# Performance work log

Hardware: AMD Instinct MI355X
Metric: run time of the kernel (lower is better)

Reference implementation:

```python
import jax, jax.numpy as jnp
import numpy as np


def _blur_kernel():
    # make_kernel([1,3,3,1]) -> outer product, normalized; * upsample_factor**2 (=4)
    k = np.array([1.0, 3.0, 3.0, 1.0], dtype=np.float32)
    k2 = np.outer(k, k)
    k2 /= k2.sum()
    k2 *= 4.0
    return jnp.asarray(k2)  # [4,4]


def setup_inputs() -> dict:
    key = jax.random.key(0)
    ks = jax.random.split(key, 6)
    B, Cin, Cout, H, W = 8, 128, 128, 128, 128
    style_dim, sd = 512, 32
    lin_out = Cin * (sd // 2) * (sd // 2)  # 128*16*16 = 32768
    return {
        "x": jax.random.normal(ks[0], (B, Cin, H, W), jnp.float32),
        "style": jax.random.normal(ks[1], (B, style_dim), jnp.float32),
        "weight": jax.random.normal(ks[2], (Cout, Cin, 3, 3), jnp.float32),
        "lin_w": jax.random.normal(ks[3], (lin_out, style_dim), jnp.float32),
        "lin_b": jnp.ones((lin_out,), jnp.float32),  # bias_init=1
        "convw_w": jax.random.normal(ks[4], (Cout, Cin, 3, 3), jnp.float32),
        "convw_b": jnp.zeros((Cout,), jnp.float32),
        "convb_w": jax.random.normal(ks[5], (Cout, Cin, 3, 3), jnp.float32),
        "convb_b": jnp.zeros((Cout,), jnp.float32),
    }


DN = ('NCHW', 'OIHW', 'NCHW')


def reference(x, style, weight, lin_w, lin_b, convw_w, convw_b, convb_w, convb_b):
    B, Cin, H, W = x.shape
    Cout, K = weight.shape[0], weight.shape[2]
    scale = 1.0 / np.sqrt(Cin * K * K)  # equalized-lr scale, fan_in = Cin*K*K
    w = scale * weight  # [Cout, Cin, K, K]; identical per-sample -> plain conv

    # F.conv_transpose2d(stride=2, padding=0) == dilated conv with flipped kernel
    out = jax.lax.conv_general_dilated(
        x, jnp.flip(w, (2, 3)), (1, 1), [(K - 1, K - 1)] * 2,
        lhs_dilation=(2, 2), dimension_numbers=DN)  # [B, Cout, 2H+1, 2W+1]

    # upfirdn2d blur with pad=(1,1): depthwise conv with flipped 4x4 kernel
    bk = _blur_kernel()
    bw = jnp.tile(jnp.flip(bk, (0, 1))[None, None], (Cout, 1, 1, 1))  # [Cout,1,4,4]
    out = jax.lax.conv_general_dilated(
        out, bw, (1, 1), [(1, 1), (1, 1)], feature_group_count=Cout,
        dimension_numbers=DN)  # [B, Cout, 2H, 2W]

    # InstanceNorm2d(affine=False), eps=1e-5, biased variance
    mu = out.mean((2, 3), keepdims=True)
    var = out.var((2, 3), keepdims=True)
    out = (out - mu) * jax.lax.rsqrt(var + 1e-5)
    Ho, Wo = out.shape[2], out.shape[3]

    # spatial_modulation_shared: EqualLinear (fused_lrelu) + View
    half = int(round(np.sqrt(lin_w.shape[0] // Cin)))  # spatial_dim // 2
    sd = 2 * half
    lscale = 1.0 / np.sqrt(style.shape[1])
    s = style @ (lin_w * lscale).T
    s = jax.nn.leaky_relu(s + lin_b, 0.2) * np.sqrt(2.0)  # fused_leaky_relu
    smap = s.reshape(B, Cin, half, half)
    # nn.Upsample(scale_factor=2, mode='nearest')
    smap = jnp.repeat(jnp.repeat(smap, 2, axis=2), 2, axis=3)  # [B,Cin,sd,sd]

    # two EqualConv2d(Cin, Cout, 3, padding=1)
    cscale = 1.0 / np.sqrt(Cin * 9)
    sw = jax.lax.conv_general_dilated(smap, convw_w * cscale, (1, 1),
                                      [(1, 1), (1, 1)], dimension_numbers=DN)
    sw = sw + convw_b[None, :, None, None]
    sb = jax.lax.conv_general_dilated(smap, convb_w * cscale, (1, 1),
                                      [(1, 1), (1, 1)], dimension_numbers=DN)
    sb = sb + convb_b[None, :, None, None]

    # F.interpolate(mode='nearest') to (Ho, Wo)
    hi = jnp.arange(Ho) * sd // Ho
    wi = jnp.arange(Wo) * sd // Wo
    sw = sw[:, :, hi][:, :, :, wi]
    sb = sb[:, :, hi][:, :, :, wi]

    return out * (1.0 + 0.3 * sw) + 0.3 * sb
```

## Files before the change

kernel.cpp:

```cpp
#include <hip/hip_runtime.h>
#include <cstdint>

#define SCALE_MAIN 0.029462782549439483f
#define LSCALE     0.044194173824159223f
#define CSCALE     0.029462782549439483f

typedef __attribute__((ext_vector_type(8))) short bf16x8;
typedef __attribute__((ext_vector_type(4))) float f32x4;
typedef __attribute__((ext_vector_type(4))) unsigned int u32x4;

static __device__ __forceinline__ float lrelu_s2(float v) {
  return (v > 0.f ? v : 0.2f * v) * 1.4142135623730951f;
}

static __device__ __forceinline__ unsigned short f2bf(float f) {
  unsigned int u = __builtin_bit_cast(unsigned int, f);
  u += 0x7FFFu + ((u >> 16) & 1u);
  return (unsigned short)(u >> 16);
}

__global__ __launch_bounds__(256) void keffb_kernel(const float* __restrict__ weight,
                                                    short* __restrict__ kb) {
  int idx = blockIdx.x * 256 + threadIdx.x;
  if (idx >= 128 * 128 * 36) return;
  int tap = idx % 9;
  int tmp = idx / 9;
  int par = tmp & 3;
  int cc  = tmp >> 2;
  int co = cc >> 7, ci = cc & 127;
  int ph = par >> 1, pw = par & 1;
  int a = tap / 3, b = tap % 3;
  int th = ph ? 3 - 2 * a : 2 - 2 * a;
  int tw = pw ? 3 - 2 * b : 2 - 2 * b;
  const float k4[4] = {1.f, 3.f, 3.f, 1.f};
  const float* wp = weight + cc * 9;
  float acc = 0.f;
  #pragma unroll
  for (int u = 0; u < 4; ++u) {
    int m = th - 1 + u;
    if (m < 0 || m > 2) continue;
    #pragma unroll
    for (int v = 0; v < 4; ++v) {
      int n = tw - 1 + v;
      if (n < 0 || n > 2) continue;
      acc += (k4[3 - u] * k4[3 - v] * (1.f / 16.f)) * wp[m * 3 + n];
    }
  }
  kb[(((par * 144) + tap * 16 + (ci >> 3)) * 128 + co) * 8 + (ci & 7)] =
      (short)f2bf(acc * SCALE_MAIN);
}

__global__ __launch_bounds__(256) void kb2_kernel(const float* __restrict__ cw_w,
                                                  const float* __restrict__ cb_w,
                                                  short* __restrict__ kb2) {
  int idx = blockIdx.x * 256 + threadIdx.x;
  if (idx >= 524288) return;
  int j   = idx & 7;
  int co  = (idx >> 3) & 255;
  int kc  = (idx >> 11) & 63;
  int par = idx >> 17;
  int k = kc * 8 + j;
  int t2 = k >> 7, ci = k & 127;
  int dy2 = t2 >> 1, dx2 = t2 & 1;
  int ph = par >> 1, pw = par & 1;
  const float* wsrc = (co < 128)
      ? cw_w + ((size_t)co * 128 + ci) * 9
      : cb_w + ((size_t)(co - 128) * 128 + ci) * 9;
  float acc = 0.f;
  #pragma unroll
  for (int kh = 0; kh < 3; ++kh) {
    bool okh = dy2 == 0 ? (ph == 0 ? kh == 0 : kh <= 1)
                        : (ph == 0 ? kh >= 1 : kh == 2);
    if (!okh) continue;
    #pragma unroll
    for (int kw = 0; kw < 3; ++kw) {
      bool okw = dx2 == 0 ? (pw == 0 ? kw == 0 : kw <= 1)
                          : (pw == 0 ? kw >= 1 : kw == 2);
      if (okw) acc += wsrc[kh * 3 + kw];
    }
  }
  kb2[idx] = (short)f2bf(acc * CSCALE);
}

__global__ __launch_bounds__(256) void xpose_kernel(const float* __restrict__ x,
                                                    unsigned short* __restrict__ xt) {
  int y = blockIdx.x, b = blockIdx.y;
  __shared__ unsigned short tl[128 * 134];
  int t = threadIdx.x;
  #pragma unroll 4
  for (int i = 0; i < 16; ++i) {
    int c = t + i * 256;
    int ci = c >> 5, x4 = c & 31;
    f32x4 v = *(const f32x4*)(x + (size_t)(b * 128 + ci) * 16384 + y * 128 + x4 * 4);
    unsigned int* dst = (unsigned int*)(tl + ci * 134 + x4 * 4);
    dst[0] = (unsigned int)f2bf(v.x) | ((unsigned int)f2bf(v.y) << 16);
    dst[1] = (unsigned int)f2bf(v.z) | ((unsigned int)f2bf(v.w) << 16);
  }
  __syncthreads();
  #pragma unroll 2
  for (int i = 0; i < 8; ++i) {
    int c = t + i * 256;
    int xcol = c >> 4, sub = c & 15;
    unsigned short u[8];
    #pragma unroll
    for (int j = 0; j < 8; ++j) u[j] = tl[(sub * 8 + j) * 134 + xcol];
    u32x4 o;
    o.x = (unsigned int)u[0] | ((unsigned int)u[1] << 16);
    o.y = (unsigned int)u[2] | ((unsigned int)u[3] << 16);
    o.z = (unsigned int)u[4] | ((unsigned int)u[5] << 16);
    o.w = (unsigned int)u[6] | ((unsigned int)u[7] << 16);
    *(u32x4*)(xt + ((size_t)(b * 128 + y) * 128 + xcol) * 128 + sub * 8) = o;
  }
}

__global__ __launch_bounds__(256) void style_kernel(const float* __restrict__ style,
                                                    const float* __restrict__ lin_w,
                                                    const float* __restrict__ lin_b,
                                                    unsigned short* __restrict__ smap_bf) {
  int wid = threadIdx.x >> 6, lane = threadIdx.x & 63;
  int gw = blockIdx.x * 4 + wid;
  const float4* st4 = (const float4*)style;
  float s[8][8];
  #pragma unroll
  for (int b = 0; b < 8; ++b) {
    float4 a0 = st4[b * 128 + lane * 2];
    float4 a1 = st4[b * 128 + lane * 2 + 1];
    s[b][0] = a0.x; s[b][1] = a0.y; s[b][2] = a0.z; s[b][3] = a0.w;
    s[b][4] = a1.x; s[b][5] = a1.y; s[b][6] = a1.z; s[b][7] = a1.w;
  }
  for (int rr = 0; rr < 16; ++rr) {
    int j = gw * 16 + rr;
    const float4* wp = (const float4*)(lin_w + (size_t)j * 512);
    float4 w0 = wp[lane * 2], w1 = wp[lane * 2 + 1];
    float acc[8];
    #pragma unroll
    for (int b = 0; b < 8; ++b) {
      acc[b] = w0.x * s[b][0] + w0.y * s[b][1] + w0.z * s[b][2] + w0.w * s[b][3]
             + w1.x * s[b][4] + w1.y * s[b][5] + w1.z * s[b][6] + w1.w * s[b][7];
    }
    #pragma unroll
    for (int m = 32; m; m >>= 1) {
      #pragma unroll
      for (int b = 0; b < 8; ++b) acc[b] += __shfl_xor(acc[b], m, 64);
    }
    if (lane == 0) {
      float bias = lin_b[j];
      int ci = j >> 8, sp = j & 255;
      #pragma unroll
      for (int b = 0; b < 8; ++b)
        smap_bf[(size_t)(b * 256 + sp) * 128 + ci] =
            f2bf(lrelu_s2(acc[b] * LSCALE + bias));
    }
  }
}

__global__ __launch_bounds__(512, 2) void modconv_kernel(
    const unsigned short* __restrict__ smap_bf, const short* __restrict__ kb2,
    const float* __restrict__ cw_b, const float* __restrict__ cb_b,
    float* __restrict__ swp) {
  extern __shared__ __align__(16) char dsm[];
  int par = blockIdx.x, b = blockIdx.y;
  int ph = par >> 1, pw = par & 1;
  int t = threadIdx.x, lane = t & 63, w = t >> 6;
  int q = w >> 1, ch = w & 1;
  int m15 = lane & 15, ksub = lane >> 4;

  for (int c = t; c < 4624; c += 512) {
    int s = c >> 4, cch = c & 15;
    int rr = s / 17, cc = s - rr * 17;
    int gr = rr - 1 + ph, gc = cc - 1 + pw;
    u32x4 v = {0u, 0u, 0u, 0u};
    if ((unsigned)gr < 16u && (unsigned)gc < 16u)
      v = *(const u32x4*)(smap_bf + ((size_t)(b * 256 + gr * 16 + gc) * 128 + cch * 8));
    int phys = (cch + s) & 15;
    *(u32x4*)(dsm + s * 256 + phys * 16) = v;
  }
  __syncthreads();

  const bf16x8* kbv = (const bf16x8*)kb2;
  f32x4 acc[4][8];
  #pragma unroll
  for (int i = 0; i < 4; ++i)
  #pragma unroll
  for (int j = 0; j < 8; ++j) acc[i][j] = (f32x4){0.f, 0.f, 0.f, 0.f};

  for (int s = 0; s < 16; ++s) {
    int t2 = s >> 2, dy2 = t2 >> 1, dx2 = t2 & 1;
    int cch = (s & 3) * 4 + ksub;
    bf16x8 av[4];
    #pragma unroll
    for (int mf = 0; mf < 4; ++mf) {
      int i = q * 4 + mf;
      int ssp = (i + dy2) * 17 + (m15 + dx2);
      int phys = (cch + ssp) & 15;
      av[mf] = *(const bf16x8*)(dsm + ssp * 256 + phys * 16);
    }
    #pragma unroll
    for (int nf = 0; nf < 8; ++nf) {
      bf16x8 bv = kbv[(size_t)((par * 64 + s * 4 + ksub) * 256 + ch * 128 + nf * 16 + m15)];
      #pragma unroll
      for (int mf = 0; mf < 4; ++mf)
        acc[mf][nf] = __builtin_amdgcn_mfma_f32_16x16x32_bf16(av[mf], bv, acc[mf][nf], 0, 0, 0);
    }
  }

  int jbase = ksub * 4;
  #pragma unroll
  for (int nf = 0; nf < 8; ++nf) {
    int co = ch * 128 + nf * 16 + m15;
    float bias = (co < 128) ? cw_b[co] : cb_b[co - 128];
    #pragma unroll
    for (int mf = 0; mf < 4; ++mf) {
      int i = q * 4 + mf;
      #pragma unroll
      for (int r = 0; r < 4; ++r) {
        int px = i * 16 + jbase + r;
        swp[((size_t)(b * 256 + co) * 4 + par) * 256 + px] = acc[mf][nf][r] + bias;
      }
    }
  }
}

#define LOADSTEP(S, AV, BV)                                                      \
  {                                                                              \
    int tap_ = (S) >> 2;                                                         \
    int ta_ = (tap_ * 11) >> 5, tb_ = tap_ - ta_ * 3;                            \
    const char* ab_ = abase + (ta_ * 66 + tb_) * 272 + ((S) & 3) * 64;           \
    _Pragma("unroll")                                                            \
    for (int mf = 0; mf < 4; ++mf) AV[mf] = *(const bf16x8*)(ab_ + mf * 4352);   \
    _Pragma("unroll")                                                            \
    for (int nf = 0; nf < 8; ++nf) BV[nf] = kbv[bbase + (S) * 512 + nf * 16];    \
  }
#define MFMASTEP(AV, BV)                                                         \
  __builtin_amdgcn_s_setprio(1);                                                 \
  _Pragma("unroll")                                                              \
  for (int nf = 0; nf < 8; ++nf)                                                 \
  _Pragma("unroll")                                                              \
  for (int mf = 0; mf < 4; ++mf)                                                 \
    acc[mf][nf] = __builtin_amdgcn_mfma_f32_16x16x32_bf16(AV[mf], BV[nf], acc[mf][nf], 0, 0, 0); \
  __builtin_amdgcn_s_setprio(0);

template <int BF16OUT>
__global__ __launch_bounds__(256, 2) void main_kernel(const unsigned short* __restrict__ xt,
    const short* __restrict__ kb, float* __restrict__ out,
    unsigned short* __restrict__ xout, float* __restrict__ partial) {
  __shared__ __align__(16) char smem[53856];
  int xh = blockIdx.x, y0 = blockIdx.y, b = blockIdx.z;
  int x0 = xh * 64;
  int t = threadIdx.x;
  int lane = t & 63, p = t >> 6;
  int m15 = lane & 15, ksub = lane >> 4;
  int ph = p >> 1, pw = p & 1;

  const char* xtc = (const char*)xt;
  for (int c = t; c < 3168; c += 256) {
    int spos = c >> 4, sub = c & 15;
    int aa = spos / 66, cc2 = spos - aa * 66;
    int y = y0 - 1 + aa, xg = x0 - 1 + cc2;
    f32x4 v = {0.f, 0.f, 0.f, 0.f};
    if ((unsigned)y < 128u && (unsigned)xg < 128u)
      v = *(const f32x4*)(xtc + ((size_t)((b * 128 + y) * 128 + xg)) * 256 + sub * 16);
    *(f32x4*)(smem + spos * 272 + sub * 16) = v;
  }
  __syncthreads();

  const bf16x8* kbv = (const bf16x8*)kb;
  int bbase = p * 18432 + ksub * 128 + m15;
  const char* abase = smem + m15 * 272 + ksub * 16;

  f32x4 acc[4][8];
  #pragma unroll
  for (int i = 0; i < 4; ++i)
  #pragma unroll
  for (int j = 0; j < 8; ++j) acc[i][j] = (f32x4){0.f, 0.f, 0.f, 0.f};

  bf16x8 avA[4], bvA[8], avB[4], bvB[8];
  LOADSTEP(0, avA, bvA)
  for (int s = 0; s < 36; s += 2) {
    LOADSTEP(s + 1, avB, bvB)
    MFMASTEP(avA, bvA)
    if (s + 2 < 36) LOADSTEP(s + 2, avA, bvA)
    MFMASTEP(avB, bvB)
  }

  __syncthreads();
  float* eps = (float*)smem;
  int co16 = t & 15, slotid = t >> 4;
  int ph2 = slotid >> 3, w16 = slotid & 7;
  #pragma unroll
  for (int r2 = 0; r2 < 4; ++r2) {
    #pragma unroll
    for (int e = 0; e < 2; ++e) {
      int nf = r2 * 2 + e;
      float s1 = 0.f, s2 = 0.f;
      #pragma unroll
      for (int mf = 0; mf < 4; ++mf)
      #pragma unroll
      for (int r = 0; r < 4; ++r) {
        int xx = mf * 16 + ksub * 4 + r;
        float v = acc[mf][nf][r];
        eps[((e * 2 + ph) * 128 + 2 * xx + pw) * 17 + m15] = v;
        s1 += v; s2 += v * v;
      }
      s1 += __shfl_xor(s1, 16, 64); s1 += __shfl_xor(s1, 32, 64);
      s2 += __shfl_xor(s2, 16, 64); s2 += __shfl_xor(s2, 32, 64);
      if (lane < 16) {
        int co = nf * 16 + lane;
        size_t pidx = (((((size_t)b * 128 + co) * 128 + y0) * 2 + xh) * 4 + p) * 2;
        partial[pidx] = s1; partial[pidx + 1] = s2;
      }
    }
    __syncthreads();
    #pragma unroll
    for (int e = 0; e < 2; ++e) {
      int nf = r2 * 2 + e;
      int co = nf * 16 + co16;
      int h = 2 * y0 + ph2;
      float vv[16];
      #pragma unroll
      for (int i = 0; i < 16; ++i)
        vv[i] = eps[((e * 2 + ph2) * 128 + w16 * 16 + i) * 17 + co16];
      size_t obase = ((size_t)(b * 128 + co) * 256 + h) * 256 + xh * 128 + w16 * 16;
      if (BF16OUT) {
        u32x4 o0, o1;
        o0.x = (unsigned int)f2bf(vv[0])  | ((unsigned int)f2bf(vv[1])  << 16);
        o0.y = (unsigned int)f2bf(vv[2])  | ((unsigned int)f2bf(vv[3])  << 16);
        o0.z = (unsigned int)f2bf(vv[4])  | ((unsigned int)f2bf(vv[5])  << 16);
        o0.w = (unsigned int)f2bf(vv[6])  | ((unsigned int)f2bf(vv[7])  << 16);
        o1.x = (unsigned int)f2bf(vv[8])  | ((unsigned int)f2bf(vv[9])  << 16);
        o1.y = (unsigned int)f2bf(vv[10]) | ((unsigned int)f2bf(vv[11]) << 16);
        o1.z = (unsigned int)f2bf(vv[12]) | ((unsigned int)f2bf(vv[13]) << 16);
        o1.w = (unsigned int)f2bf(vv[14]) | ((unsigned int)f2bf(vv[15]) << 16);
        *(u32x4*)(xout + obase) = o0;
        *(u32x4*)(xout + obase + 8) = o1;
      } else {
        #pragma unroll
        for (int i = 0; i < 4; ++i) {
          f32x4 o4 = {vv[i * 4], vv[i * 4 + 1], vv[i * 4 + 2], vv[i * 4 + 3]};
          *(f32x4*)(out + obase + i * 4) = o4;
        }
      }
    }
    __syncthreads();
  }
}

__global__ __launch_bounds__(256) void stats_kernel(const float* __restrict__ partial,
                                                    float* __restrict__ stats) {
  int bc = blockIdx.x;
  int t = threadIdx.x;
  float s1 = 0.f, s2 = 0.f;
  for (int j = t; j < 1024; j += 256) {
    s1 += partial[(size_t)bc * 2048 + 2 * j];
    s2 += partial[(size_t)bc * 2048 + 2 * j + 1];
  }
  #pragma unroll
  for (int m = 32; m; m >>= 1) { s1 += __shfl_xor(s1, m, 64); s2 += __shfl_xor(s2, m, 64); }
  __shared__ float rb[8];
  if ((t & 63) == 0) { rb[(t >> 6) * 2] = s1; rb[(t >> 6) * 2 + 1] = s2; }
  __syncthreads();
  if (t == 0) {
    float a1 = rb[0] + rb[2] + rb[4] + rb[6];
    float a2 = rb[1] + rb[3] + rb[5] + rb[7];
    float mean = a1 * (1.f / 65536.f);
    float var = a2 * (1.f / 65536.f) - mean * mean;
    stats[bc * 2] = mean;
    stats[bc * 2 + 1] = rsqrtf(var + 1e-5f);
  }
}

__global__ __launch_bounds__(256) void final_kernel(float* __restrict__ out,
    const float* __restrict__ swp, const float* __restrict__ stats) {
  unsigned int tid = blockIdx.x * 256 + threadIdx.x;
  unsigned int e = tid * 4;
  unsigned int w = e & 255u;
  unsigned int h = (e >> 8) & 255u;
  unsigned int bc = e >> 16;
  unsigned int b = bc >> 7, co = bc & 127u;
  float mean = stats[bc * 2], rstd = stats[bc * 2 + 1];
  unsigned int r32 = h >> 3, c32 = w >> 3;
  unsigned int par = (r32 & 1u) * 2 + (c32 & 1u);
  unsigned int px = (r32 >> 1) * 16 + (c32 >> 1);
  float msw = swp[((size_t)(b * 256 + co) * 4 + par) * 256 + px];
  float msb = swp[((size_t)(b * 256 + 128 + co) * 4 + par) * 256 + px];
  float f1 = (1.f + 0.3f * msw) * rstd;
  float f0 = 0.3f * msb - mean * f1;
  float4 v = *(float4*)(out + e);
  v.x = v.x * f1 + f0;
  v.y = v.y * f1 + f0;
  v.z = v.z * f1 + f0;
  v.w = v.w * f1 + f0;
  *(float4*)(out + e) = v;
}

__global__ __launch_bounds__(256) void final_bf16_kernel(float* __restrict__ out,
    const unsigned short* __restrict__ xout,
    const float* __restrict__ swp, const float* __restrict__ stats) {
  unsigned int tid = blockIdx.x * 256 + threadIdx.x;
  unsigned int e = tid * 8;
  unsigned int w = e & 255u;
  unsigned int h = (e >> 8) & 255u;
  unsigned int bc = e >> 16;
  unsigned int b = bc >> 7, co = bc & 127u;
  float mean = stats[bc * 2], rstd = stats[bc * 2 + 1];
  unsigned int r32 = h >> 3, c32 = w >> 3;
  unsigned int par = (r32 & 1u) * 2 + (c32 & 1u);
  unsigned int px = (r32 >> 1) * 16 + (c32 >> 1);
  float msw = swp[((size_t)(b * 256 + co) * 4 + par) * 256 + px];
  float msb = swp[((size_t)(b * 256 + 128 + co) * 4 + par) * 256 + px];
  float f1 = (1.f + 0.3f * msw) * rstd;
  float f0 = 0.3f * msb - mean * f1;
  u32x4 uv = *(const u32x4*)(xout + e);
  float o[8];
  #pragma unroll
  for (int j = 0; j < 4; ++j) {
    unsigned int word = uv[j];
    float lo = __builtin_bit_cast(float, word << 16);
    float hi = __builtin_bit_cast(float, word & 0xFFFF0000u);
    o[2 * j]     = lo * f1 + f0;
    o[2 * j + 1] = hi * f1 + f0;
  }
  f32x4 a = {o[0], o[1], o[2], o[3]}, c = {o[4], o[5], o[6], o[7]};
  *(f32x4*)(out + e) = a;
  *(f32x4*)(out + e + 4) = c;
}

extern "C" void kernel_launch(void* const* d_in, const int* in_sizes, int n_in,
                              void* d_out, int out_size, void* d_ws, size_t ws_size,
                              hipStream_t stream) {
  const float* x      = (const float*)d_in[0];
  const float* style  = (const float*)d_in[1];
  const float* weight = (const float*)d_in[2];
  const float* lin_w  = (const float*)d_in[3];
  const float* lin_b  = (const float*)d_in[4];
  const float* cw_w   = (const float*)d_in[5];
  const float* cw_b   = (const float*)d_in[6];
  const float* cb_w   = (const float*)d_in[7];
  const float* cb_b   = (const float*)d_in[8];
  float* out = (float*)d_out;
  char* ws = (char*)d_ws;

  short*          kbb     = (short*)(ws);
  unsigned short* xt      = (unsigned short*)(ws + 1179648);
  float*          swp     = (float*)(ws + 34734080);
  float*          part    = (float*)(ws + 43122688);
  short*          kb2     = (short*)(ws + 43122688);
  unsigned short* smap_bf = (unsigned short*)(ws + 44171264);
  float*          stats   = (float*)(ws + 51511296);
  unsigned short* xout    = (unsigned short*)(ws + 51519488);
  bool bigws = ws_size >= (size_t)186785792;

  keffb_kernel<<<dim3(2304), dim3(256), 0, stream>>>(weight, kbb);
  kb2_kernel<<<dim3(2048), dim3(256), 0, stream>>>(cw_w, cb_w, kb2);
  xpose_kernel<<<dim3(128, 8), dim3(256), 0, stream>>>(x, xt);
  style_kernel<<<dim3(512), dim3(256), 0, stream>>>(style, lin_w, lin_b, smap_bf);
  modconv_kernel<<<dim3(4, 8), dim3(512), 73984, stream>>>(smap_bf, kb2, cw_b, cb_b, swp);
  if (bigws) {
    main_kernel<1><<<dim3(2, 128, 8), dim3(256), 0, stream>>>(xt, kbb, out, xout, part);
    stats_kernel<<<dim3(1024), dim3(256), 0, stream>>>(part, stats);
    final_bf16_kernel<<<dim3(32768), dim3(256), 0, stream>>>(out, xout, swp, stats);
  } else {
    main_kernel<0><<<dim3(2, 128, 8), dim3(256), 0, stream>>>(xt, kbb, out, nullptr, part);
    stats_kernel<<<dim3(1024), dim3(256), 0, stream>>>(part, stats);
    final_kernel<<<dim3(65536), dim3(256), 0, stream>>>(out, swp, stats);
  }
}
```

Baseline: 343.8 us.

## Split transposed conv and blur into separate kernels with bf16 intermediate and fused prep

Replaces the blur-folded 4x4-effective-weight main GEMM (36 k-steps per parity) with a plain 3x3 transposed-conv GEMM over 9 taps (4 k-steps each), writing an unblurred bf16 intermediate per parity plane. A new blur kernel then applies the separable [1,3,3,1] filter from shared memory, running twice: once to accumulate instance-norm statistics and once to recompute the blur and apply norm plus spatial modulation directly into the output. The four prep kernels are merged into one launch. This cuts MFMA work and removes the fp32 out round-trip, at the cost of recomputing the blur and rereading the intermediate twice.

```diff
diff --git a/kernel.cpp b/kernel.cpp
--- a/kernel.cpp
+++ b/kernel.cpp
@@ -12,144 +12,128 @@
 static __device__ __forceinline__ float lrelu_s2(float v) {
   return (v > 0.f ? v : 0.2f * v) * 1.4142135623730951f;
 }
-
 static __device__ __forceinline__ unsigned short f2bf(float f) {
   unsigned int u = __builtin_bit_cast(unsigned int, f);
   u += 0x7FFFu + ((u >> 16) & 1u);
   return (unsigned short)(u >> 16);
 }
-
-__global__ __launch_bounds__(256) void keffb_kernel(const float* __restrict__ weight,
-                                                    short* __restrict__ kb) {
-  int idx = blockIdx.x * 256 + threadIdx.x;
-  if (idx >= 128 * 128 * 36) return;
-  int tap = idx % 9;
-  int tmp = idx / 9;
-  int par = tmp & 3;
-  int cc  = tmp >> 2;
-  int co = cc >> 7, ci = cc & 127;
-  int ph = par >> 1, pw = par & 1;
-  int a = tap / 3, b = tap % 3;
-  int th = ph ? 3 - 2 * a : 2 - 2 * a;
-  int tw = pw ? 3 - 2 * b : 2 - 2 * b;
-  const float k4[4] = {1.f, 3.f, 3.f, 1.f};
-  const float* wp = weight + cc * 9;
-  float acc = 0.f;
-  #pragma unroll
-  for (int u = 0; u < 4; ++u) {
-    int m = th - 1 + u;
-    if (m < 0 || m > 2) continue;
-    #pragma unroll
-    for (int v = 0; v < 4; ++v) {
-      int n = tw - 1 + v;
-      if (n < 0 || n > 2) continue;
-      acc += (k4[3 - u] * k4[3 - v] * (1.f / 16.f)) * wp[m * 3 + n];
-    }
-  }
-  kb[(((par * 144) + tap * 16 + (ci >> 3)) * 128 + co) * 8 + (ci & 7)] =
-      (short)f2bf(acc * SCALE_MAIN);
-}
-
-__global__ __launch_bounds__(256) void kb2_kernel(const float* __restrict__ cw_w,
-                                                  const float* __restrict__ cb_w,
-                                                  short* __restrict__ kb2) {
-  int idx = blockIdx.x * 256 + threadIdx.x;
-  if (idx >= 524288) return;
-  int j   = idx & 7;
-  int co  = (idx >> 3) & 255;
-  int kc  = (idx >> 11) & 63;
-  int par = idx >> 17;
-  int k = kc * 8 + j;
-  int t2 = k >> 7, ci = k & 127;
-  int dy2 = t2 >> 1, dx2 = t2 & 1;
-  int ph = par >> 1, pw = par & 1;
-  const float* wsrc = (co < 128)
-      ? cw_w + ((size_t)co * 128 + ci) * 9
-      : cb_w + ((size_t)(co - 128) * 128 + ci) * 9;
-  float acc = 0.f;
-  #pragma unroll
-  for (int kh = 0; kh < 3; ++kh) {
-    bool okh = dy2 == 0 ? (ph == 0 ? kh == 0 : kh <= 1)
-                        : (ph == 0 ? kh >= 1 : kh == 2);
-    if (!okh) continue;
-    #pragma unroll
-    for (int kw = 0; kw < 3; ++kw) {
-      bool okw = dx2 == 0 ? (pw == 0 ? kw == 0 : kw <= 1)
-                          : (pw == 0 ? kw >= 1 : kw == 2);
-      if (okw) acc += wsrc[kh * 3 + kw];
-    }
-  }
-  kb2[idx] = (short)f2bf(acc * CSCALE);
-}
-
-__global__ __launch_bounds__(256) void xpose_kernel(const float* __restrict__ x,
-                                                    unsigned short* __restrict__ xt) {
-  int y = blockIdx.x, b = blockIdx.y;
-  __shared__ unsigned short tl[128 * 134];
+static __device__ __forceinline__ float s2f(unsigned short s) {
+  return __builtin_bit_cast(float, (unsigned int)s << 16);
+}
+
+__global__ __launch_bounds__(256) void prep_all(
+    const float* __restrict__ weight, const float* __restrict__ cw_w,
+    const float* __restrict__ cb_w, const float* __restrict__ x,
+    const float* __restrict__ style, const float* __restrict__ lin_w,
+    const float* __restrict__ lin_b, short* __restrict__ kbu,
+    short* __restrict__ kb2, unsigned short* __restrict__ xt,
+    unsigned short* __restrict__ smap_bf) {
+  int bid = blockIdx.x;
   int t = threadIdx.x;
-  #pragma unroll 4
-  for (int i = 0; i < 16; ++i) {
-    int c = t + i * 256;
-    int ci = c >> 5, x4 = c & 31;
-    f32x4 v = *(const f32x4*)(x + (size_t)(b * 128 + ci) * 16384 + y * 128 + x4 * 4);
-    unsigned int* dst = (unsigned int*)(tl + ci * 134 + x4 * 4);
-    dst[0] = (unsigned int)f2bf(v.x) | ((unsigned int)f2bf(v.y) << 16);
-    dst[1] = (unsigned int)f2bf(v.z) | ((unsigned int)f2bf(v.w) << 16);
-  }
-  __syncthreads();
-  #pragma unroll 2
-  for (int i = 0; i < 8; ++i) {
-    int c = t + i * 256;
-    int xcol = c >> 4, sub = c & 15;
-    unsigned short u[8];
-    #pragma unroll
-    for (int j = 0; j < 8; ++j) u[j] = tl[(sub * 8 + j) * 134 + xcol];
-    u32x4 o;
-    o.x = (unsigned int)u[0] | ((unsigned int)u[1] << 16);
-    o.y = (unsigned int)u[2] | ((unsigned int)u[3] << 16);
-    o.z = (unsigned int)u[4] | ((unsigned int)u[5] << 16);
-    o.w = (unsigned int)u[6] | ((unsigned int)u[7] << 16);
-    *(u32x4*)(xt + ((size_t)(b * 128 + y) * 128 + xcol) * 128 + sub * 8) = o;
-  }
-}
-
-__global__ __launch_bounds__(256) void style_kernel(const float* __restrict__ style,
-                                                    const float* __restrict__ lin_w,
-                                                    const float* __restrict__ lin_b,
-                                                    unsigned short* __restrict__ smap_bf) {
-  int wid = threadIdx.x >> 6, lane = threadIdx.x & 63;
-  int gw = blockIdx.x * 4 + wid;
-  const float4* st4 = (const float4*)style;
-  float s[8][8];
-  #pragma unroll
-  for (int b = 0; b < 8; ++b) {
-    float4 a0 = st4[b * 128 + lane * 2];
-    float4 a1 = st4[b * 128 + lane * 2 + 1];
-    s[b][0] = a0.x; s[b][1] = a0.y; s[b][2] = a0.z; s[b][3] = a0.w;
-    s[b][4] = a1.x; s[b][5] = a1.y; s[b][6] = a1.z; s[b][7] = a1.w;
-  }
-  for (int rr = 0; rr < 16; ++rr) {
-    int j = gw * 16 + rr;
-    const float4* wp = (const float4*)(lin_w + (size_t)j * 512);
-    float4 w0 = wp[lane * 2], w1 = wp[lane * 2 + 1];
-    float acc[8];
+  if (bid < 2048) {
+    int idx = bid * 256 + t;
+    int j   = idx & 7;
+    int co  = (idx >> 3) & 255;
+    int kc  = (idx >> 11) & 63;
+    int par = idx >> 17;
+    int k = kc * 8 + j;
+    int t2 = k >> 7, ci = k & 127;
+    int dy2 = t2 >> 1, dx2 = t2 & 1;
+    int ph = par >> 1, pw = par & 1;
+    const float* wsrc = (co < 128)
+        ? cw_w + ((size_t)co * 128 + ci) * 9
+        : cb_w + ((size_t)(co - 128) * 128 + ci) * 9;
+    float acc = 0.f;
+    #pragma unroll
+    for (int kh = 0; kh < 3; ++kh) {
+      bool okh = dy2 == 0 ? (ph == 0 ? kh == 0 : kh <= 1)
+                          : (ph == 0 ? kh >= 1 : kh == 2);
+      if (!okh) continue;
+      #pragma unroll
+      for (int kw = 0; kw < 3; ++kw) {
+        bool okw = dx2 == 0 ? (pw == 0 ? kw == 0 : kw <= 1)
+                            : (pw == 0 ? kw >= 1 : kw == 2);
+        if (okw) acc += wsrc[kh * 3 + kw];
+      }
+    }
+    kb2[idx] = (short)f2bf(acc * CSCALE);
+  } else if (bid < 2624) {
+    int idx2 = (bid - 2048) * 256 + t;
+    int j    = idx2 & 7;
+    int co   = (idx2 >> 3) & 127;
+    int ksub = (idx2 >> 10) & 3;
+    int s    = (idx2 >> 12) & 3;
+    int tp   = idx2 >> 14;
+    int ci = s * 32 + ksub * 8 + j;
+    int wr = (tp == 0 || tp == 1 || tp == 4) ? 2
+           : (tp >= 6) ? 1 : 0;
+    int wc = (tp == 0 || tp == 2 || tp == 6) ? 2
+           : (tp == 4 || tp == 5 || tp == 8) ? 1 : 0;
+    float v = weight[((size_t)(co * 128 + ci)) * 9 + wr * 3 + wc] * SCALE_MAIN;
+    kbu[idx2] = (short)f2bf(v);
+  } else if (bid < 3648) {
+    int q = bid - 2624;
+    int y = q & 127, b = q >> 7;
+    __shared__ unsigned short tl[128 * 134];
+    #pragma unroll 4
+    for (int i = 0; i < 16; ++i) {
+      int c = t + i * 256;
+      int ci = c >> 5, x4 = c & 31;
+      f32x4 v = *(const f32x4*)(x + (size_t)(b * 128 + ci) * 16384 + y * 128 + x4 * 4);
+      unsigned int* dst = (unsigned int*)(tl + ci * 134 + x4 * 4);
+      dst[0] = (unsigned int)f2bf(v.x) | ((unsigned int)f2bf(v.y) << 16);
+      dst[1] = (unsigned int)f2bf(v.z) | ((unsigned int)f2bf(v.w) << 16);
+    }
+    __syncthreads();
+    #pragma unroll 2
+    for (int i = 0; i < 8; ++i) {
+      int c = t + i * 256;
+      int xcol = c >> 4, sub = c & 15;
+      unsigned short u[8];
+      #pragma unroll
+      for (int j = 0; j < 8; ++j) u[j] = tl[(sub * 8 + j) * 134 + xcol];
+      u32x4 o;
+      o.x = (unsigned int)u[0] | ((unsigned int)u[1] << 16);
+      o.y = (unsigned int)u[2] | ((unsigned int)u[3] << 16);
+      o.z = (unsigned int)u[4] | ((unsigned int)u[5] << 16);
+      o.w = (unsigned int)u[6] | ((unsigned int)u[7] << 16);
+      *(u32x4*)(xt + ((size_t)(b * 128 + y) * 128 + xcol) * 128 + sub * 8) = o;
+    }
+  } else {
+    int wid = t >> 6, lane = t & 63;
+    int gw = (bid - 3648) * 4 + wid;
+    const float4* st4 = (const float4*)style;
+    float s[8][8];
     #pragma unroll
     for (int b = 0; b < 8; ++b) {
-      acc[b] = w0.x * s[b][0] + w0.y * s[b][1] + w0.z * s[b][2] + w0.w * s[b][3]
-             + w1.x * s[b][4] + w1.y * s[b][5] + w1.z * s[b][6] + w1.w * s[b][7];
-    }
-    #pragma unroll
-    for (int m = 32; m; m >>= 1) {
-      #pragma unroll
-      for (int b = 0; b < 8; ++b) acc[b] += __shfl_xor(acc[b], m, 64);
-    }
-    if (lane == 0) {
-      float bias = lin_b[j];
-      int ci = j >> 8, sp = j & 255;
-      #pragma unroll
-      for (int b = 0; b < 8; ++b)
-        smap_bf[(size_t)(b * 256 + sp) * 128 + ci] =
-            f2bf(lrelu_s2(acc[b] * LSCALE + bias));
+      float4 a0 = st4[b * 128 + lane * 2];
+      float4 a1 = st4[b * 128 + lane * 2 + 1];
+      s[b][0] = a0.x; s[b][1] = a0.y; s[b][2] = a0.z; s[b][3] = a0.w;
+      s[b][4] = a1.x; s[b][5] = a1.y; s[b][6] = a1.z; s[b][7] = a1.w;
+    }
+    for (int rr = 0; rr < 16; ++rr) {
+      int j = gw * 16 + rr;
+      const float4* wp = (const float4*)(lin_w + (size_t)j * 512);
+      float4 w0 = wp[lane * 2], w1 = wp[lane * 2 + 1];
+      float acc[8];
+      #pragma unroll
+      for (int b = 0; b < 8; ++b) {
+        acc[b] = w0.x * s[b][0] + w0.y * s[b][1] + w0.z * s[b][2] + w0.w * s[b][3]
+               + w1.x * s[b][4] + w1.y * s[b][5] + w1.z * s[b][6] + w1.w * s[b][7];
+      }
+      #pragma unroll
+      for (int m = 32; m; m >>= 1) {
+        #pragma unroll
+        for (int b = 0; b < 8; ++b) acc[b] += __shfl_xor(acc[b], m, 64);
+      }
+      if (lane == 0) {
+        float bias = lin_b[j];
+        int ci = j >> 8, sp = j & 255;
+        #pragma unroll
+        for (int b = 0; b < 8; ++b)
+          smap_bf[(size_t)(b * 256 + sp) * 128 + ci] =
+              f2bf(lrelu_s2(acc[b] * LSCALE + bias));
+      }
     }
   }
 }
@@ -221,42 +205,22 @@
   }
 }
 
-#define LOADSTEP(S, AV, BV)                                                      \
-  {                                                                              \
-    int tap_ = (S) >> 2;                                                         \
-    int ta_ = (tap_ * 11) >> 5, tb_ = tap_ - ta_ * 3;                            \
-    const char* ab_ = abase + (ta_ * 66 + tb_) * 272 + ((S) & 3) * 64;           \
-    _Pragma("unroll")                                                            \
-    for (int mf = 0; mf < 4; ++mf) AV[mf] = *(const bf16x8*)(ab_ + mf * 4352);   \
-    _Pragma("unroll")                                                            \
-    for (int nf = 0; nf < 8; ++nf) BV[nf] = kbv[bbase + (S) * 512 + nf * 16];    \
-  }
-#define MFMASTEP(AV, BV)                                                         \
-  __builtin_amdgcn_s_setprio(1);                                                 \
-  _Pragma("unroll")                                                              \
-  for (int nf = 0; nf < 8; ++nf)                                                 \
-  _Pragma("unroll")                                                              \
-  for (int mf = 0; mf < 4; ++mf)                                                 \
-    acc[mf][nf] = __builtin_amdgcn_mfma_f32_16x16x32_bf16(AV[mf], BV[nf], acc[mf][nf], 0, 0, 0); \
-  __builtin_amdgcn_s_setprio(0);
-
-template <int BF16OUT>
-__global__ __launch_bounds__(256, 2) void main_kernel(const unsigned short* __restrict__ xt,
-    const short* __restrict__ kb, float* __restrict__ out,
-    unsigned short* __restrict__ xout, float* __restrict__ partial) {
-  __shared__ __align__(16) char smem[53856];
-  int xh = blockIdx.x, y0 = blockIdx.y, b = blockIdx.z;
-  int x0 = xh * 64;
-  int t = threadIdx.x;
-  int lane = t & 63, p = t >> 6;
+__global__ __launch_bounds__(576) void convt_kernel(
+    const unsigned short* __restrict__ xt, const short* __restrict__ kbu,
+    unsigned short* __restrict__ out1) {
+  extern __shared__ __align__(16) char dsm2[];
+  char* smem = dsm2;
+  float* eps = (float*)(dsm2 + 26928);
+  int cg = blockIdx.x, rp = blockIdx.y, b = blockIdx.z;
+  int r0 = rp * 2, c0 = cg * 32;
+  int t = threadIdx.x, lane = t & 63, w = t >> 6;
   int m15 = lane & 15, ksub = lane >> 4;
-  int ph = p >> 1, pw = p & 1;
 
   const char* xtc = (const char*)xt;
-  for (int c = t; c < 3168; c += 256) {
+  for (int c = t; c < 1584; c += 576) {
     int spos = c >> 4, sub = c & 15;
-    int aa = spos / 66, cc2 = spos - aa * 66;
-    int y = y0 - 1 + aa, xg = x0 - 1 + cc2;
+    int lr = spos / 33, lc = spos - lr * 33;
+    int y = r0 - 1 + lr, xg = c0 - 1 + lc;
     f32x4 v = {0.f, 0.f, 0.f, 0.f};
     if ((unsigned)y < 128u && (unsigned)xg < 128u)
       v = *(const f32x4*)(xtc + ((size_t)((b * 128 + y) * 128 + xg)) * 256 + sub * 16);
@@ -264,9 +228,15 @@
   }
   __syncthreads();
 
-  const bf16x8* kbv = (const bf16x8*)kb;
-  int bbase = p * 18432 + ksub * 128 + m15;
-  const char* abase = smem + m15 * 272 + ksub * 16;
+  int du = (w == 0 || w == 1 || w == 4) ? -1 : 0;
+  int dv = (w == 0 || w == 2 || w == 6) ? -1 : 0;
+  const char* abase[4];
+  #pragma unroll
+  for (int mf = 0; mf < 4; ++mf)
+    abase[mf] = smem + (((mf >> 1) + du + 1) * 33 + (mf & 1) * 16 + m15 + dv + 1) * 272
+              + ksub * 16;
+  const bf16x8* kbv = (const bf16x8*)kbu;
+  int bb = w * 2048 + ksub * 128 + m15;
 
   f32x4 acc[4][8];
   #pragma unroll
@@ -274,155 +244,148 @@
   #pragma unroll
   for (int j = 0; j < 8; ++j) acc[i][j] = (f32x4){0.f, 0.f, 0.f, 0.f};
 
-  bf16x8 avA[4], bvA[8], avB[4], bvB[8];
-  LOADSTEP(0, avA, bvA)
-  for (int s = 0; s < 36; s += 2) {
-    LOADSTEP(s + 1, avB, bvB)
-    MFMASTEP(avA, bvA)
-    if (s + 2 < 36) LOADSTEP(s + 2, avA, bvA)
-    MFMASTEP(avB, bvB)
-  }
+  auto LD = [&](int s, bf16x8* av, bf16x8* bv) {
+    #pragma unroll
+    for (int mf = 0; mf < 4; ++mf) av[mf] = *(const bf16x8*)(abase[mf] + s * 64);
+    #pragma unroll
+    for (int nf = 0; nf < 8; ++nf) bv[nf] = kbv[bb + s * 512 + nf * 16];
+  };
+  auto MM = [&](bf16x8* av, bf16x8* bv) {
+    #pragma unroll
+    for (int nf = 0; nf < 8; ++nf)
+    #pragma unroll
+    for (int mf = 0; mf < 4; ++mf)
+      acc[mf][nf] = __builtin_amdgcn_mfma_f32_16x16x32_bf16(av[mf], bv[nf], acc[mf][nf], 0, 0, 0);
+  };
+  bf16x8 aA[4], bA[8], aB[4], bB[8];
+  LD(0, aA, bA); LD(1, aB, bB);
+  MM(aA, bA);    LD(2, aA, bA);
+  MM(aB, bB);    LD(3, aB, bB);
+  MM(aA, bA);    MM(aB, bB);
 
   __syncthreads();
-  float* eps = (float*)smem;
-  int co16 = t & 15, slotid = t >> 4;
-  int ph2 = slotid >> 3, w16 = slotid & 7;
-  #pragma unroll
-  for (int r2 = 0; r2 < 4; ++r2) {
-    #pragma unroll
-    for (int e = 0; e < 2; ++e) {
-      int nf = r2 * 2 + e;
-      float s1 = 0.f, s2 = 0.f;
-      #pragma unroll
-      for (int mf = 0; mf < 4; ++mf)
-      #pragma unroll
-      for (int r = 0; r < 4; ++r) {
-        int xx = mf * 16 + ksub * 4 + r;
-        float v = acc[mf][nf][r];
-        eps[((e * 2 + ph) * 128 + 2 * xx + pw) * 17 + m15] = v;
-        s1 += v; s2 += v * v;
-      }
-      s1 += __shfl_xor(s1, 16, 64); s1 += __shfl_xor(s1, 32, 64);
-      s2 += __shfl_xor(s2, 16, 64); s2 += __shfl_xor(s2, 32, 64);
-      if (lane < 16) {
-        int co = nf * 16 + lane;
-        size_t pidx = (((((size_t)b * 128 + co) * 128 + y0) * 2 + xh) * 4 + p) * 2;
-        partial[pidx] = s1; partial[pidx + 1] = s2;
-      }
-    }
+  for (int nf = 0; nf < 8; ++nf) {
+    #pragma unroll
+    for (int mf = 0; mf < 4; ++mf)
+    #pragma unroll
+    for (int r = 0; r < 4; ++r)
+      eps[(w * 64 + mf * 16 + ksub * 4 + r) * 17 + m15] = acc[mf][nf][r];
     __syncthreads();
-    #pragma unroll
-    for (int e = 0; e < 2; ++e) {
-      int nf = r2 * 2 + e;
-      int co = nf * 16 + co16;
-      int h = 2 * y0 + ph2;
-      float vv[16];
-      #pragma unroll
-      for (int i = 0; i < 16; ++i)
-        vv[i] = eps[((e * 2 + ph2) * 128 + w16 * 16 + i) * 17 + co16];
-      size_t obase = ((size_t)(b * 128 + co) * 256 + h) * 256 + xh * 128 + w16 * 16;
-      if (BF16OUT) {
-        u32x4 o0, o1;
-        o0.x = (unsigned int)f2bf(vv[0])  | ((unsigned int)f2bf(vv[1])  << 16);
-        o0.y = (unsigned int)f2bf(vv[2])  | ((unsigned int)f2bf(vv[3])  << 16);
-        o0.z = (unsigned int)f2bf(vv[4])  | ((unsigned int)f2bf(vv[5])  << 16);
-        o0.w = (unsigned int)f2bf(vv[6])  | ((unsigned int)f2bf(vv[7])  << 16);
-        o1.x = (unsigned int)f2bf(vv[8])  | ((unsigned int)f2bf(vv[9])  << 16);
-        o1.y = (unsigned int)f2bf(vv[10]) | ((unsigned int)f2bf(vv[11]) << 16);
-        o1.z = (unsigned int)f2bf(vv[12]) | ((unsigned int)f2bf(vv[13]) << 16);
-        o1.w = (unsigned int)f2bf(vv[14]) | ((unsigned int)f2bf(vv[15]) << 16);
-        *(u32x4*)(xout + obase) = o0;
-        *(u32x4*)(xout + obase + 8) = o1;
-      } else {
-        #pragma unroll
-        for (int i = 0; i < 4; ++i) {
-          f32x4 o4 = {vv[i * 4], vv[i * 4 + 1], vv[i * 4 + 2], vv[i * 4 + 3]};
-          *(f32x4*)(out + obase + i * 4) = o4;
-        }
-      }
+    for (int idx = t; idx < 4096; idx += 576) {
+      int c5 = idx & 31, co16 = (idx >> 5) & 15;
+      int prow = (idx >> 9) & 1, pl = idx >> 10;
+      int px = prow * 32 + c5;
+      int start = (pl == 0) ? 0 : (pl == 1) ? 4 : (pl == 2) ? 6 : 8;
+      int cnt   = (pl == 0) ? 4 : (pl == 3) ? 1 : 2;
+      float v = 0.f;
+      for (int k = 0; k < cnt; ++k)
+        v += eps[((start + k) * 64 + px) * 17 + co16];
+      int r = r0 + prow, cc = c0 + c5, co = nf * 16 + co16;
+      if (cc < 129)
+        out1[((((size_t)(b * 4 + pl) * 128 + co) * 130 + r) * 132 + cc)] = f2bf(v);
     }
     __syncthreads();
   }
 }
 
-__global__ __launch_bounds__(256) void stats_kernel(const float* __restrict__ partial,
-                                                    float* __restrict__ stats) {
-  int bc = blockIdx.x;
-  int t = threadIdx.x;
+template <int PASS>
+__global__ __launch_bounds__(256) void blur_kernel(
+    const unsigned short* __restrict__ out1, float* __restrict__ part,
+    const float* __restrict__ swp, float* __restrict__ dout) {
+  __shared__ unsigned short S[4][34][36];
+  __shared__ float T[64 * 2 * 34];
+  __shared__ float msh[2];
+  __shared__ float rb2[8];
+  int bx = blockIdx.x;
+  int tt = bx & 3, ss = bx >> 2;
+  int co = blockIdx.y, b = blockIdx.z;
+  int t = threadIdx.x, lane = t & 63, wid = t >> 6;
+  int bc = b * 128 + co;
+
+  if (PASS == 1 && t == 0) {
+    float s1 = 0.f, s2 = 0.f;
+    #pragma unroll
+    for (int i = 0; i < 16; ++i) {
+      s1 += part[((size_t)bc * 16 + i) * 2];
+      s2 += part[((size_t)bc * 16 + i) * 2 + 1];
+    }
+    float mean = s1 * (1.f / 65536.f);
+    float var = s2 * (1.f / 65536.f) - mean * mean;
+    msh[0] = mean; msh[1] = rsqrtf(var + 1e-5f);
+  }
+
+  int rb = 32 * ss - 1, cb = 32 * tt - 2;
+  for (int i = t; i < 2448; i += 256) {
+    int pl = i / 612, rem = i - pl * 612;
+    int lr = rem / 18, cp = rem - lr * 18;
+    int r = rb + lr, c = cb + cp * 2;
+    int Rp = (pl < 2) ? 129 : 128;
+    int Cp = (pl & 1) ? 128 : 129;
+    const unsigned short* base = out1 + (((size_t)(b * 4 + pl) * 128 + co) * 130 + r) * 132;
+    unsigned int v = 0u;
+    if ((unsigned)r < (unsigned)Rp) {
+      if (c >= 0 && c + 1 < Cp) v = *(const unsigned int*)(base + c);
+      else {
+        unsigned int lo = ((unsigned)c < (unsigned)Cp) ? base[c] : 0u;
+        unsigned int hi = ((unsigned)(c + 1) < (unsigned)Cp) ? base[c + 1] : 0u;
+        v = lo | (hi << 16);
+      }
+    }
+    *(unsigned int*)(&S[pl][lr][cp * 2]) = v;
+  }
+  __syncthreads();
+
+  for (int i = t; i < 4352; i += 256) {
+    int hl = i / 68, rem = i - hl * 68;
+    int pw = rem / 34, cl = rem - pw * 34;
+    int lrb = (hl + 1) >> 1;
+    int E = pw, O = 2 + pw;
+    float v;
+    if (hl & 1)
+      v = s2f(S[E][lrb][cl + 1]) + 3.f * s2f(S[O][lrb][cl + 1])
+        + 3.f * s2f(S[E][lrb + 1][cl + 1]) + s2f(S[O][lrb + 1][cl + 1]);
+    else
+      v = s2f(S[O][lrb][cl + 1]) + 3.f * s2f(S[E][lrb + 1][cl + 1])
+        + 3.f * s2f(S[O][lrb + 1][cl + 1]) + s2f(S[E][lrb + 2][cl + 1]);
+    T[(hl * 2 + pw) * 34 + cl] = v;
+  }
+  __syncthreads();
+
+  float mean = 0.f, rstd = 0.f;
+  if (PASS == 1) { mean = msh[0]; rstd = msh[1]; }
   float s1 = 0.f, s2 = 0.f;
-  for (int j = t; j < 1024; j += 256) {
-    s1 += partial[(size_t)bc * 2048 + 2 * j];
-    s2 += partial[(size_t)bc * 2048 + 2 * j + 1];
-  }
-  #pragma unroll
-  for (int m = 32; m; m >>= 1) { s1 += __shfl_xor(s1, m, 64); s2 += __shfl_xor(s2, m, 64); }
-  __shared__ float rb[8];
-  if ((t & 63) == 0) { rb[(t >> 6) * 2] = s1; rb[(t >> 6) * 2 + 1] = s2; }
-  __syncthreads();
-  if (t == 0) {
-    float a1 = rb[0] + rb[2] + rb[4] + rb[6];
-    float a2 = rb[1] + rb[3] + rb[5] + rb[7];
-    float mean = a1 * (1.f / 65536.f);
-    float var = a2 * (1.f / 65536.f) - mean * mean;
-    stats[bc * 2] = mean;
-    stats[bc * 2 + 1] = rsqrtf(var + 1e-5f);
-  }
-}
-
-__global__ __launch_bounds__(256) void final_kernel(float* __restrict__ out,
-    const float* __restrict__ swp, const float* __restrict__ stats) {
-  unsigned int tid = blockIdx.x * 256 + threadIdx.x;
-  unsigned int e = tid * 4;
-  unsigned int w = e & 255u;
-  unsigned int h = (e >> 8) & 255u;
-  unsigned int bc = e >> 16;
-  unsigned int b = bc >> 7, co = bc & 127u;
-  float mean = stats[bc * 2], rstd = stats[bc * 2 + 1];
-  unsigned int r32 = h >> 3, c32 = w >> 3;
-  unsigned int par = (r32 & 1u) * 2 + (c32 & 1u);
-  unsigned int px = (r32 >> 1) * 16 + (c32 >> 1);
-  float msw = swp[((size_t)(b * 256 + co) * 4 + par) * 256 + px];
-  float msb = swp[((size_t)(b * 256 + 128 + co) * 4 + par) * 256 + px];
-  float f1 = (1.f + 0.3f * msw) * rstd;
-  float f0 = 0.3f * msb - mean * f1;
-  float4 v = *(float4*)(out + e);
-  v.x = v.x * f1 + f0;
-  v.y = v.y * f1 + f0;
-  v.z = v.z * f1 + f0;
-  v.w = v.w * f1 + f0;
-  *(float4*)(out + e) = v;
-}
-
-__global__ __launch_bounds__(256) void final_bf16_kernel(float* __restrict__ out,
-    const unsigned short* __restrict__ xout,
-    const float* __restrict__ swp, const float* __restrict__ stats) {
-  unsigned int tid = blockIdx.x * 256 + threadIdx.x;
-  unsigned int e = tid * 8;
-  unsigned int w = e & 255u;
-  unsigned int h = (e >> 8) & 255u;
-  unsigned int bc = e >> 16;
-  unsigned int b = bc >> 7, co = bc & 127u;
-  float mean = stats[bc * 2], rstd = stats[bc * 2 + 1];
-  unsigned int r32 = h >> 3, c32 = w >> 3;
-  unsigned int par = (r32 & 1u) * 2 + (c32 & 1u);
-  unsigned int px = (r32 >> 1) * 16 + (c32 >> 1);
-  float msw = swp[((size_t)(b * 256 + co) * 4 + par) * 256 + px];
-  float msb = swp[((size_t)(b * 256 + 128 + co) * 4 + par) * 256 + px];
-  float f1 = (1.f + 0.3f * msw) * rstd;
-  float f0 = 0.3f * msb - mean * f1;
-  u32x4 uv = *(const u32x4*)(xout + e);
-  float o[8];
-  #pragma unroll
-  for (int j = 0; j < 4; ++j) {
-    unsigned int word = uv[j];
-    float lo = __builtin_bit_cast(float, word << 16);
-    float hi = __builtin_bit_cast(float, word & 0xFFFF0000u);
-    o[2 * j]     = lo * f1 + f0;
-    o[2 * j + 1] = hi * f1 + f0;
-  }
-  f32x4 a = {o[0], o[1], o[2], o[3]}, c = {o[4], o[5], o[6], o[7]};
-  *(f32x4*)(out + e) = a;
-  *(f32x4*)(out + e + 4) = c;
+  for (int i = t; i < 4096; i += 256) {
+    int hl = i >> 6, wl = i & 63;
+    int lcb = (wl + 1) >> 1;
+    const float* T0 = &T[hl * 68];
+    const float* T1 = T0 + 34;
+    float v;
+    if (wl & 1) v = T0[lcb] + 3.f * T1[lcb] + 3.f * T0[lcb + 1] + T1[lcb + 1];
+    else        v = T1[lcb] + 3.f * T0[lcb + 1] + 3.f * T1[lcb + 1] + T0[lcb + 2];
+    v *= 0.0625f;
+    if (PASS == 0) {
+      s1 += v; s2 += v * v;
+    } else {
+      int h = 64 * ss + hl, wg = 64 * tt + wl;
+      int par = ((h >> 3) & 1) * 2 + ((wg >> 3) & 1);
+      int px2 = (h >> 4) * 16 + (wg >> 4);
+      float msw = swp[((size_t)(b * 256 + co) * 4 + par) * 256 + px2];
+      float msb = swp[((size_t)(b * 256 + 128 + co) * 4 + par) * 256 + px2];
+      float f1 = (1.f + 0.3f * msw) * rstd;
+      float f0 = 0.3f * msb - mean * f1;
+      dout[((size_t)bc * 256 + h) * 256 + wg] = v * f1 + f0;
+    }
+  }
+  if (PASS == 0) {
+    #pragma unroll
+    for (int m = 32; m; m >>= 1) { s1 += __shfl_xor(s1, m, 64); s2 += __shfl_xor(s2, m, 64); }
+    if (lane == 0) { rb2[wid * 2] = s1; rb2[wid * 2 + 1] = s2; }
+    __syncthreads();
+    if (t == 0) {
+      part[((size_t)bc * 16 + bx) * 2]     = rb2[0] + rb2[2] + rb2[4] + rb2[6];
+      part[((size_t)bc * 16 + bx) * 2 + 1] = rb2[1] + rb2[3] + rb2[5] + rb2[7];
+    }
+  }
 }
 
 extern "C" void kernel_launch(void* const* d_in, const int* in_sizes, int n_in,
@@ -440,28 +403,18 @@
   float* out = (float*)d_out;
   char* ws = (char*)d_ws;
 
-  short*          kbb     = (short*)(ws);
-  unsigned short* xt      = (unsigned short*)(ws + 1179648);
-  float*          swp     = (float*)(ws + 34734080);
-  float*          part    = (float*)(ws + 43122688);
-  short*          kb2     = (short*)(ws + 43122688);
-  unsigned short* smap_bf = (unsigned short*)(ws + 44171264);
-  float*          stats   = (float*)(ws + 51511296);
-  unsigned short* xout    = (unsigned short*)(ws + 51519488);
-  bool bigws = ws_size >= (size_t)186785792;
-
-  keffb_kernel<<<dim3(2304), dim3(256), 0, stream>>>(weight, kbb);
-  kb2_kernel<<<dim3(2048), dim3(256), 0, stream>>>(cw_w, cb_w, kb2);
-  xpose_kernel<<<dim3(128, 8), dim3(256), 0, stream>>>(x, xt);
-  style_kernel<<<dim3(512), dim3(256), 0, stream>>>(style, lin_w, lin_b, smap_bf);
+  short*          kbu     = (short*)(ws);
+  short*          kb2     = (short*)(ws + 294912);
+  unsigned short* xt      = (unsigned short*)(ws + 1343488);
+  unsigned short* smap_bf = (unsigned short*)(ws + 34897920);
+  float*          swp     = (float*)(ws + 35422208);
+  float*          part    = (float*)(ws + 43810816);
+  unsigned short* out1    = (unsigned short*)(ws + 43941888);
+
+  prep_all<<<dim3(4160), dim3(256), 0, stream>>>(
+      weight, cw_w, cb_w, x, style, lin_w, lin_b, kbu, kb2, xt, smap_bf);
   modconv_kernel<<<dim3(4, 8), dim3(512), 73984, stream>>>(smap_bf, kb2, cw_b, cb_b, swp);
-  if (bigws) {
-    main_kernel<1><<<dim3(2, 128, 8), dim3(256), 0, stream>>>(xt, kbb, out, xout, part);
-    stats_kernel<<<dim3(1024), dim3(256), 0, stream>>>(part, stats);
-    final_bf16_kernel<<<dim3(32768), dim3(256), 0, stream>>>(out, xout, swp, stats);
-  } else {
-    main_kernel<0><<<dim3(2, 128, 8), dim3(256), 0, stream>>>(xt, kbb, out, nullptr, part);
-    stats_kernel<<<dim3(1024), dim3(256), 0, stream>>>(part, stats);
-    final_kernel<<<dim3(65536), dim3(256), 0, stream>>>(out, swp, stats);
-  }
-}
+  convt_kernel<<<dim3(5, 65, 8), dim3(576), 66096, stream>>>(xt, kbu, out1);
+  blur_kernel<0><<<dim3(16, 128, 8), dim3(256), 0, stream>>>(out1, part, swp, out);
+  blur_kernel<1><<<dim3(16, 128, 8), dim3(256), 0, stream>>>(out1, part, swp, out);
+}
```

New measurement: 804.2 us. 2.34x slower.
